# Optimization experiments

Measured on AMD Instinct MI355X. Metric: run time of the kernel, lower is better.

## Reference

```python
import jax, jax.numpy as jnp
import numpy as np

FEATURE_SIZE = (64, 64)   # (H, W)
N_REGIONS = 32
POOL = (3, 3)             # (ph, pw)
IOU_THR = 0.4
B, R, C = 4, 128, 256


def setup_inputs() -> dict:
    key = jax.random.key(0)
    kf, kx, ky, kw, kh = jax.random.split(key, 5)
    H, W = FEATURE_SIZE
    features = jax.random.normal(kf, (B, H, W, C), dtype=jnp.float32)
    # realistic RPN-style proposals in feature coordinates (x, y, w, h)
    x = jax.random.uniform(kx, (B, R), minval=0.0, maxval=W - 4.0)
    y = jax.random.uniform(ky, (B, R), minval=0.0, maxval=H - 4.0)
    w = jax.random.uniform(kw, (B, R), minval=4.0, maxval=W / 2.0)
    h = jax.random.uniform(kh, (B, R), minval=4.0, maxval=H / 2.0)
    roi = jnp.stack([x, y, w, h], axis=-1).astype(jnp.float32)
    return {"features": features, "roi": roi}


def _pairwise_iou(b):
    # b: [R, 4] xywh
    x1, y1 = b[:, 0], b[:, 1]
    x2, y2 = x1 + b[:, 2], y1 + b[:, 3]
    area = b[:, 2] * b[:, 3]
    iw = jnp.maximum(jnp.minimum(x2[:, None], x2[None, :]) - jnp.maximum(x1[:, None], x1[None, :]), 0.0)
    ih = jnp.maximum(jnp.minimum(y2[:, None], y2[None, :]) - jnp.maximum(y1[:, None], y1[None, :]), 0.0)
    inter = iw * ih
    return inter / (area[:, None] + area[None, :] - inter)


def _nms_indices(iou):
    # greedy sequential suppression: a discarded box never suppresses others
    Rn = iou.shape[0]
    j = jnp.arange(Rn)

    def body(p, keep):
        sup = keep & (j > p) & (iou[p] > IOU_THR) & keep[p]
        return keep & ~sup

    keep = jax.lax.fori_loop(0, Rn - 1, body, jnp.ones((Rn,), bool))
    # kept indices in ascending (objectness) order, padded with last index
    idx = jnp.sort(jnp.where(keep, j, Rn))[:N_REGIONS]
    return jnp.minimum(idx, Rn - 1).astype(jnp.int32)


def _clip_roi(roi):
    # roi: [B, N, 4] float xywh -> int32 [B, N, 4] xywh, clipped + min-size fixed
    H, W = FEATURE_SIZE
    x_min = jnp.maximum(0.0, roi[..., 0]).astype(jnp.int32)
    y_min = jnp.maximum(0.0, roi[..., 1]).astype(jnp.int32)
    x_max = jnp.minimum(float(W), roi[..., 0] + roi[..., 2]).astype(jnp.int32)
    y_max = jnp.minimum(float(H), roi[..., 1] + roi[..., 3]).astype(jnp.int32)

    def fix_axis(mn, mx, ps, fs):
        pad = ps - (mx - mn)
        fix_min = mn < pad // 2
        fix_max = fs - mx < (1 + pad) // 2
        sym = (pad > 0) & ~(fix_min | fix_max)
        omin = jnp.where(sym, mn - pad // 2, mn)
        omax = jnp.where(sym, mx + (1 + pad) // 2, mx)
        cmn = (pad > 0) & fix_min
        cmx = (pad > 0) & fix_max
        omin = jnp.where(cmn, 0, omin)
        omax = jnp.where(cmn, ps, omax)
        omin = jnp.where(cmx, fs - ps, omin)
        omax = jnp.where(cmx, fs, omax)
        return omin, omax

    xmn, xmx = fix_axis(x_min, x_max, POOL[1], W)
    ymn, ymx = fix_axis(y_min, y_max, POOL[0], H)
    return jnp.stack([xmn, ymn, xmx - xmn, ymx - ymn], axis=-1)


def _pool_one(feat, box):
    # feat: [H, W, C]; box: int32 [4] = (x, y, w, h); adaptive max pool to POOL
    H, W = FEATURE_SIZE
    ph, pw = POOL
    x, y, w, h = box[0], box[1], box[2], box[3]
    rows = jnp.arange(H)
    cols = jnp.arange(W)
    # cell index per row/col; last cell absorbs the remainder (matches floor steps)
    rcell = jnp.clip((rows - y) // (h // ph), 0, ph - 1)
    ccell = jnp.clip((cols - x) // (w // pw), 0, pw - 1)
    rvalid = (rows >= y) & (rows < y + h)
    cvalid = (cols >= x) & (cols < x + w)
    neg = jnp.finfo(feat.dtype).min
    f = jnp.where(rvalid[:, None, None], feat, neg)           # [H, W, C]
    rmax = jax.ops.segment_max(f, rcell, num_segments=ph)     # [ph, W, C]
    rmax = jnp.where(cvalid[None, :, None], rmax, neg)
    out = jax.ops.segment_max(jnp.swapaxes(rmax, 0, 1), ccell, num_segments=pw)  # [pw, ph, C]
    return jnp.swapaxes(out, 0, 1)                            # [ph, pw, C]


def reference(features, roi):
    iou = jax.vmap(_pairwise_iou)(roi)                         # [B, R, R]
    idx = jax.vmap(_nms_indices)(iou)                          # [B, N]
    roi_sup = jnp.take_along_axis(roi, idx[:, :, None], axis=1)  # [B, N, 4]
    roi_clipped = _clip_roi(roi_sup)                           # int32 [B, N, 4]
    pool_img = jax.vmap(_pool_one, in_axes=(None, 0))          # over regions
    pooled = jax.vmap(pool_img, in_axes=(0, 0))(features, roi_clipped)  # [B, N, ph, pw, C]
    return pooled, roi_clipped
```

## Files before the change

kernel.cpp:

```cpp
#include <hip/hip_runtime.h>
#include <float.h>

#define FH 64
#define FW 64
#define FC 256
#define NB 4
#define NR 128
#define NREG 32
#define POOLH 3
#define POOLW 3
#define IOU_THR 0.4f
#define NCELL (POOLH * POOLW)
#define MAXPIX 160

#define POOLED_ELEMS (NB * NREG * NCELL * FC)

__device__ inline void fix_axis(int mn, int mx, int ps, int fs, int& omin, int& omax) {
    int pad = ps - (mx - mn);
    bool fix_min = mn < (pad >> 1);
    bool fix_max = (fs - mx) < ((1 + pad) >> 1);
    bool sym = (pad > 0) && !(fix_min || fix_max);
    omin = sym ? (mn - (pad >> 1)) : mn;
    omax = sym ? (mx + ((1 + pad) >> 1)) : mx;
    if ((pad > 0) && fix_min) { omin = 0; omax = ps; }
    if ((pad > 0) && fix_max) { omin = fs - ps; omax = fs; }
}

__device__ inline float4 max4(float4 a, float4 b) {
    float4 o;
    o.x = fmaxf(a.x, b.x); o.y = fmaxf(a.y, b.y);
    o.z = fmaxf(a.z, b.z); o.w = fmaxf(a.w, b.w);
    return o;
}

__device__ inline unsigned long long readlane64(unsigned long long v, int lane) {
    unsigned lo = (unsigned)__builtin_amdgcn_readlane((int)(unsigned)v, lane);
    unsigned hi = (unsigned)__builtin_amdgcn_readlane((int)(unsigned)(v >> 32), lane);
    return ((unsigned long long)hi << 32) | lo;
}

__global__ __launch_bounds__(256) void fused_kernel(
    const float* __restrict__ features,
    const float* __restrict__ roi,
    float* __restrict__ out)
{
    const int hwid = blockIdx.x;
    const int b = (hwid >> 1) & 3;
    const int j = (hwid >> 3) * 2 + (hwid & 1);
    const int r = j / NCELL;
    const int cell = j - r * NCELL;
    const int ci = cell / POOLW, cj = cell - ci * POOLW;
    const int reg = b * NREG + r;
    const int tid = threadIdx.x;
    const int wid = tid >> 6;
    const int lane = tid & 63;

    __shared__ float sx1[NR], sy1[NR], sx2[NR], sy2[NR], sarea[NR];
    __shared__ unsigned long long smask[NR][2];
    __shared__ int spix[MAXPIX];
    __shared__ float4 sred[4][64];

    if (tid < NR) {
        const float4 bx = *(const float4*)(roi + ((size_t)b * NR + tid) * 4);
        sx1[tid] = bx.x; sy1[tid] = bx.y;
        sx2[tid] = bx.x + bx.z; sy2[tid] = bx.y + bx.w;
        sarea[tid] = bx.z * bx.w;
    }
    __syncthreads();

    if (wid != 1) {
        const int p = tid & 127;
        const int half = tid >> 7;
        const int j0 = half << 6;
        const float px1 = sx1[p], py1 = sy1[p], px2 = sx2[p], py2 = sy2[p], pa = sarea[p];
        unsigned long long m = 0ull;
        #pragma unroll 8
        for (int t = 0; t < 64; ++t) {
            const int jj = j0 + t;
            float iw = fmaxf(fminf(px2, sx2[jj]) - fmaxf(px1, sx1[jj]), 0.0f);
            float ih = fmaxf(fminf(py2, sy2[jj]) - fmaxf(py1, sy1[jj]), 0.0f);
            float inter = iw * ih;
            bool sup = (jj > p) && (inter > IOU_THR * (pa + sarea[jj] - inter));
            m |= ((unsigned long long)sup) << t;
        }
        smask[p][half] = m;
    }
    __syncthreads();

    const unsigned long long aLo = smask[lane][0];
    const unsigned long long aHi = smask[lane][1];
    const unsigned long long bHi = smask[lane + 64][1];

    int idx = NR - 1;
    {
        unsigned long long k1 = ~0ull;
        int cnt = 0;
        unsigned long long cur = ~0ull;
        while (cur && cnt < NREG) {
            int p = __ffsll((unsigned long long)cur) - 1;
            if (cnt == r) idx = p;
            ++cnt;
            int ps = __builtin_amdgcn_readfirstlane(p);
            unsigned long long m0 = readlane64(aLo, ps);
            unsigned long long m1 = readlane64(aHi, ps);
            cur = (cur & (cur - 1)) & ~m0;
            k1 &= ~m1;
        }
        cur = k1;
        while (cur && cnt < NREG) {
            int p = __ffsll((unsigned long long)cur) - 1;
            if (cnt == r) idx = 64 + p;
            ++cnt;
            int ps = __builtin_amdgcn_readfirstlane(p);
            unsigned long long m1 = readlane64(bHi, ps);
            cur = (cur & (cur - 1)) & ~m1;
        }
    }

    int xmn, xmx, ymn, ymx;
    {
        float x1 = sx1[idx], y1 = sy1[idx], x2f = sx2[idx], y2f = sy2[idx];
        int x_min = (int)fmaxf(0.0f, x1);
        int y_min = (int)fmaxf(0.0f, y1);
        int x_max = (int)fminf((float)FW, x2f);
        int y_max = (int)fminf((float)FH, y2f);
        fix_axis(x_min, x_max, POOLW, FW, xmn, xmx);
        fix_axis(y_min, y_max, POOLH, FH, ymn, ymx);
    }
    if (tid == 0 && cell == 0) {
        float* orc = out + POOLED_ELEMS + ((size_t)reg) * 4;
        orc[0] = (float)xmn;
        orc[1] = (float)ymn;
        orc[2] = (float)(xmx - xmn);
        orc[3] = (float)(ymx - ymn);
    }

    const int x = xmn, y = ymn, w = xmx - xmn, h = ymx - ymn;
    const int hh = h / POOLH;
    const int ww = w / POOLW;
    const int r0 = y + ci * hh;
    const int r1 = (ci < POOLH - 1) ? (y + (ci + 1) * hh) : (y + h);
    const int c0 = x + cj * ww;
    const int c1 = (cj < POOLW - 1) ? (x + (cj + 1) * ww) : (x + w);
    const int ncols = c1 - c0;
    const int n = (r1 - r0) * ncols;

    if (tid < n) {
        int q = tid / ncols;
        int cc = tid - q * ncols;
        spix[tid] = ((r0 + q) * FW + (c0 + cc)) * FC;
    }
    __syncthreads();

    const float* fbase = features + (size_t)b * FH * FW * FC;
    const float4 negv = {-FLT_MAX, -FLT_MAX, -FLT_MAX, -FLT_MAX};
    float4 m0 = negv, m1 = negv, m2 = negv, m3 = negv;
    float4 m4 = negv, m5 = negv, m6 = negv, m7 = negv;
    int k = wid;
    for (; k + 28 < n; k += 32) {
        int o0 = spix[k],      o1 = spix[k + 4],  o2 = spix[k + 8],  o3 = spix[k + 12];
        int o4 = spix[k + 16], o5 = spix[k + 20], o6 = spix[k + 24], o7 = spix[k + 28];
        float4 v0 = ((const float4*)(fbase + o0))[lane];
        float4 v1 = ((const float4*)(fbase + o1))[lane];
        float4 v2 = ((const float4*)(fbase + o2))[lane];
        float4 v3 = ((const float4*)(fbase + o3))[lane];
        float4 v4 = ((const float4*)(fbase + o4))[lane];
        float4 v5 = ((const float4*)(fbase + o5))[lane];
        float4 v6 = ((const float4*)(fbase + o6))[lane];
        float4 v7 = ((const float4*)(fbase + o7))[lane];
        m0 = max4(m0, v0); m1 = max4(m1, v1); m2 = max4(m2, v2); m3 = max4(m3, v3);
        m4 = max4(m4, v4); m5 = max4(m5, v5); m6 = max4(m6, v6); m7 = max4(m7, v7);
    }
    for (; k + 12 < n; k += 16) {
        int o0 = spix[k], o1 = spix[k + 4], o2 = spix[k + 8], o3 = spix[k + 12];
        float4 v0 = ((const float4*)(fbase + o0))[lane];
        float4 v1 = ((const float4*)(fbase + o1))[lane];
        float4 v2 = ((const float4*)(fbase + o2))[lane];
        float4 v3 = ((const float4*)(fbase + o3))[lane];
        m0 = max4(m0, v0); m1 = max4(m1, v1); m2 = max4(m2, v2); m3 = max4(m3, v3);
    }
    for (; k < n; k += 4) {
        float4 v = ((const float4*)(fbase + spix[k]))[lane];
        m0 = max4(m0, v);
    }
    m0 = max4(max4(m0, m1), max4(m2, m3));
    m4 = max4(max4(m4, m5), max4(m6, m7));
    sred[wid][lane] = max4(m0, m4);
    __syncthreads();

    if (tid < 64) {
        float4 a = max4(max4(sred[0][tid], sred[1][tid]),
                        max4(sred[2][tid], sred[3][tid]));
        float4* ob = (float4*)(out + ((size_t)reg * NCELL + cell) * FC);
        ob[tid] = a;
    }
}

extern "C" void kernel_launch(void* const* d_in, const int* in_sizes, int n_in,
                              void* d_out, int out_size, void* d_ws, size_t ws_size,
                              hipStream_t stream) {
    const float* features = (const float*)d_in[0];
    const float* roi = (const float*)d_in[1];
    float* out = (float*)d_out;
    (void)in_sizes; (void)n_in; (void)out_size; (void)d_ws; (void)ws_size;

    fused_kernel<<<NB * NREG * NCELL, 256, 0, stream>>>(features, roi, out);
}
```

Before: 82.00 us.

## Assign one pooling cell per wavefront and cut grid to 256 blocks

The kernel moves from one block per (region, cell), where all four wavefronts split that cell's pixels, to one pooling cell per wavefront, with 64 blocks per image. This cuts the number of blocks that redundantly recompute the IoU mask and NMS from 1152 to 256. Wave 0 now resolves all 32 kept boxes at once and stores the clipped boxes in shared memory. The 32 leftover cells per image go to wave 0 of the first 32 blocks. This adds load imbalance, since each wave reduces a whole cell with a 16-way unrolled gather, and occupancy falls from four times as many blocks.

```diff
diff --git a/kernel.cpp b/kernel.cpp
--- a/kernel.cpp
+++ b/kernel.cpp
@@ -11,7 +11,7 @@
 #define POOLW 3
 #define IOU_THR 0.4f
 #define NCELL (POOLH * POOLW)
-#define MAXPIX 160
+#define MAXPIX 144
 
 #define POOLED_ELEMS (NB * NREG * NCELL * FC)
 
@@ -39,7 +39,69 @@
     return ((unsigned long long)hi << 32) | lo;
 }
 
-__global__ __launch_bounds__(256) void fused_kernel(
+__device__ inline float4 pool_pixels(const float* __restrict__ fbase,
+                                     const int* spixw, int nn, int lane) {
+    const float4 negv = {-FLT_MAX, -FLT_MAX, -FLT_MAX, -FLT_MAX};
+    float4 m[16];
+    #pragma unroll
+    for (int i = 0; i < 16; ++i) m[i] = negv;
+    int k = 0;
+    for (; k + 15 < nn; k += 16) {
+        float4 v[16];
+        #pragma unroll
+        for (int i = 0; i < 16; ++i)
+            v[i] = ((const float4*)(fbase + spixw[k + i]))[lane];
+        #pragma unroll
+        for (int i = 0; i < 16; ++i) m[i] = max4(m[i], v[i]);
+    }
+    for (; k + 3 < nn; k += 4) {
+        float4 v0 = ((const float4*)(fbase + spixw[k]))[lane];
+        float4 v1 = ((const float4*)(fbase + spixw[k + 1]))[lane];
+        float4 v2 = ((const float4*)(fbase + spixw[k + 2]))[lane];
+        float4 v3 = ((const float4*)(fbase + spixw[k + 3]))[lane];
+        m[0] = max4(m[0], v0); m[1] = max4(m[1], v1);
+        m[2] = max4(m[2], v2); m[3] = max4(m[3], v3);
+    }
+    for (; k < nn; ++k)
+        m[0] = max4(m[0], ((const float4*)(fbase + spixw[k]))[lane]);
+    #pragma unroll
+    for (int s = 8; s > 0; s >>= 1)
+        for (int i = 0; i < s; ++i) m[i] = max4(m[i], m[i + s]);
+    return m[0];
+}
+
+__device__ inline void do_cell(int c, int b, const int (*sbox4)[4], int* spixw,
+                               const float* __restrict__ fbase,
+                               float* __restrict__ out, int lane) {
+    const int r = c / NCELL;
+    const int cell = c - r * NCELL;
+    const int ci = cell / POOLW, cj = cell - ci * POOLW;
+    const int x = sbox4[r][0], y = sbox4[r][1], w = sbox4[r][2], h = sbox4[r][3];
+    const int hh = h / POOLH;
+    const int ww = w / POOLW;
+    const int r0 = y + ci * hh;
+    const int r1 = (ci < POOLH - 1) ? (y + (ci + 1) * hh) : (y + h);
+    const int c0 = x + cj * ww;
+    const int c1 = (cj < POOLW - 1) ? (x + (cj + 1) * ww) : (x + w);
+    const int ncols = c1 - c0;
+    const int nn = (r1 - r0) * ncols;
+
+    for (int t = lane; t < nn; t += 64) {
+        int q = t / ncols;
+        int cc = t - q * ncols;
+        spixw[t] = ((r0 + q) * FW + (c0 + cc)) * FC;
+    }
+
+    float4 a = pool_pixels(fbase, spixw, nn, lane);
+    ((float4*)(out + ((size_t)(b * NREG + r) * NCELL + cell) * FC))[lane] = a;
+
+    if (cell == 0 && lane < 4) {
+        int v = (lane == 0) ? x : (lane == 1) ? y : (lane == 2) ? w : h;
+        out[POOLED_ELEMS + (size_t)(b * NREG + r) * 4 + lane] = (float)v;
+    }
+}
+
+__global__ __launch_bounds__(256, 1) void fused_kernel(
     const float* __restrict__ features,
     const float* __restrict__ roi,
     float* __restrict__ out)
@@ -47,18 +109,15 @@
     const int hwid = blockIdx.x;
     const int b = (hwid >> 1) & 3;
     const int j = (hwid >> 3) * 2 + (hwid & 1);
-    const int r = j / NCELL;
-    const int cell = j - r * NCELL;
-    const int ci = cell / POOLW, cj = cell - ci * POOLW;
-    const int reg = b * NREG + r;
     const int tid = threadIdx.x;
     const int wid = tid >> 6;
     const int lane = tid & 63;
+    const int g = j * 4 + wid;
 
     __shared__ float sx1[NR], sy1[NR], sx2[NR], sy2[NR], sarea[NR];
     __shared__ unsigned long long smask[NR][2];
-    __shared__ int spix[MAXPIX];
-    __shared__ float4 sred[4][64];
+    __shared__ int sbox4[NREG][4];
+    __shared__ int spix[4][MAXPIX];
 
     if (tid < NR) {
         const float4 bx = *(const float4*)(roi + ((size_t)b * NR + tid) * 4);
@@ -87,113 +146,54 @@
     }
     __syncthreads();
 
-    const unsigned long long aLo = smask[lane][0];
-    const unsigned long long aHi = smask[lane][1];
-    const unsigned long long bHi = smask[lane + 64][1];
-
-    int idx = NR - 1;
-    {
-        unsigned long long k1 = ~0ull;
-        int cnt = 0;
-        unsigned long long cur = ~0ull;
-        while (cur && cnt < NREG) {
-            int p = __ffsll((unsigned long long)cur) - 1;
-            if (cnt == r) idx = p;
-            ++cnt;
-            int ps = __builtin_amdgcn_readfirstlane(p);
-            unsigned long long m0 = readlane64(aLo, ps);
-            unsigned long long m1 = readlane64(aHi, ps);
-            cur = (cur & (cur - 1)) & ~m0;
-            k1 &= ~m1;
+    if (wid == 0) {
+        const unsigned long long aLo = smask[lane][0];
+        const unsigned long long aHi = smask[lane][1];
+        const unsigned long long bHi = smask[lane + 64][1];
+
+        int myidx = NR - 1;
+        {
+            unsigned long long k1 = ~0ull;
+            int cnt = 0;
+            unsigned long long cur = ~0ull;
+            while (cur && cnt < NREG) {
+                int p = __ffsll((unsigned long long)cur) - 1;
+                if (cnt == lane) myidx = p;
+                ++cnt;
+                int ps = __builtin_amdgcn_readfirstlane(p);
+                cur = (cur & (cur - 1)) & ~readlane64(aLo, ps);
+                k1 &= ~readlane64(aHi, ps);
+            }
+            cur = k1;
+            while (cur && cnt < NREG) {
+                int p = __ffsll((unsigned long long)cur) - 1;
+                if (cnt == lane) myidx = 64 + p;
+                ++cnt;
+                int ps = __builtin_amdgcn_readfirstlane(p);
+                cur = (cur & (cur - 1)) & ~readlane64(bHi, ps);
+            }
         }
-        cur = k1;
-        while (cur && cnt < NREG) {
-            int p = __ffsll((unsigned long long)cur) - 1;
-            if (cnt == r) idx = 64 + p;
-            ++cnt;
-            int ps = __builtin_amdgcn_readfirstlane(p);
-            unsigned long long m1 = readlane64(bHi, ps);
-            cur = (cur & (cur - 1)) & ~m1;
+        if (lane < NREG) {
+            float x1 = sx1[myidx], y1 = sy1[myidx], x2f = sx2[myidx], y2f = sy2[myidx];
+            int x_min = (int)fmaxf(0.0f, x1);
+            int y_min = (int)fmaxf(0.0f, y1);
+            int x_max = (int)fminf((float)FW, x2f);
+            int y_max = (int)fminf((float)FH, y2f);
+            int xmn, xmx, ymn, ymx;
+            fix_axis(x_min, x_max, POOLW, FW, xmn, xmx);
+            fix_axis(y_min, y_max, POOLH, FH, ymn, ymx);
+            sbox4[lane][0] = xmn;
+            sbox4[lane][1] = ymn;
+            sbox4[lane][2] = xmx - xmn;
+            sbox4[lane][3] = ymx - ymn;
         }
     }
-
-    int xmn, xmx, ymn, ymx;
-    {
-        float x1 = sx1[idx], y1 = sy1[idx], x2f = sx2[idx], y2f = sy2[idx];
-        int x_min = (int)fmaxf(0.0f, x1);
-        int y_min = (int)fmaxf(0.0f, y1);
-        int x_max = (int)fminf((float)FW, x2f);
-        int y_max = (int)fminf((float)FH, y2f);
-        fix_axis(x_min, x_max, POOLW, FW, xmn, xmx);
-        fix_axis(y_min, y_max, POOLH, FH, ymn, ymx);
-    }
-    if (tid == 0 && cell == 0) {
-        float* orc = out + POOLED_ELEMS + ((size_t)reg) * 4;
-        orc[0] = (float)xmn;
-        orc[1] = (float)ymn;
-        orc[2] = (float)(xmx - xmn);
-        orc[3] = (float)(ymx - ymn);
-    }
-
-    const int x = xmn, y = ymn, w = xmx - xmn, h = ymx - ymn;
-    const int hh = h / POOLH;
-    const int ww = w / POOLW;
-    const int r0 = y + ci * hh;
-    const int r1 = (ci < POOLH - 1) ? (y + (ci + 1) * hh) : (y + h);
-    const int c0 = x + cj * ww;
-    const int c1 = (cj < POOLW - 1) ? (x + (cj + 1) * ww) : (x + w);
-    const int ncols = c1 - c0;
-    const int n = (r1 - r0) * ncols;
-
-    if (tid < n) {
-        int q = tid / ncols;
-        int cc = tid - q * ncols;
-        spix[tid] = ((r0 + q) * FW + (c0 + cc)) * FC;
-    }
     __syncthreads();
 
     const float* fbase = features + (size_t)b * FH * FW * FC;
-    const float4 negv = {-FLT_MAX, -FLT_MAX, -FLT_MAX, -FLT_MAX};
-    float4 m0 = negv, m1 = negv, m2 = negv, m3 = negv;
-    float4 m4 = negv, m5 = negv, m6 = negv, m7 = negv;
-    int k = wid;
-    for (; k + 28 < n; k += 32) {
-        int o0 = spix[k],      o1 = spix[k + 4],  o2 = spix[k + 8],  o3 = spix[k + 12];
-        int o4 = spix[k + 16], o5 = spix[k + 20], o6 = spix[k + 24], o7 = spix[k + 28];
-        float4 v0 = ((const float4*)(fbase + o0))[lane];
-        float4 v1 = ((const float4*)(fbase + o1))[lane];
-        float4 v2 = ((const float4*)(fbase + o2))[lane];
-        float4 v3 = ((const float4*)(fbase + o3))[lane];
-        float4 v4 = ((const float4*)(fbase + o4))[lane];
-        float4 v5 = ((const float4*)(fbase + o5))[lane];
-        float4 v6 = ((const float4*)(fbase + o6))[lane];
-        float4 v7 = ((const float4*)(fbase + o7))[lane];
-        m0 = max4(m0, v0); m1 = max4(m1, v1); m2 = max4(m2, v2); m3 = max4(m3, v3);
-        m4 = max4(m4, v4); m5 = max4(m5, v5); m6 = max4(m6, v6); m7 = max4(m7, v7);
-    }
-    for (; k + 12 < n; k += 16) {
-        int o0 = spix[k], o1 = spix[k + 4], o2 = spix[k + 8], o3 = spix[k + 12];
-        float4 v0 = ((const float4*)(fbase + o0))[lane];
-        float4 v1 = ((const float4*)(fbase + o1))[lane];
-        float4 v2 = ((const float4*)(fbase + o2))[lane];
-        float4 v3 = ((const float4*)(fbase + o3))[lane];
-        m0 = max4(m0, v0); m1 = max4(m1, v1); m2 = max4(m2, v2); m3 = max4(m3, v3);
-    }
-    for (; k < n; k += 4) {
-        float4 v = ((const float4*)(fbase + spix[k]))[lane];
-        m0 = max4(m0, v);
-    }
-    m0 = max4(max4(m0, m1), max4(m2, m3));
-    m4 = max4(max4(m4, m5), max4(m6, m7));
-    sred[wid][lane] = max4(m0, m4);
-    __syncthreads();
-
-    if (tid < 64) {
-        float4 a = max4(max4(sred[0][tid], sred[1][tid]),
-                        max4(sred[2][tid], sred[3][tid]));
-        float4* ob = (float4*)(out + ((size_t)reg * NCELL + cell) * FC);
-        ob[tid] = a;
-    }
+    do_cell(g, b, sbox4, spix[wid], fbase, out, lane);
+    if (wid == 0 && j < NREG)
+        do_cell(256 + j, b, sbox4, spix[0], fbase, out, lane);
 }
 
 extern "C" void kernel_launch(void* const* d_in, const int* in_sizes, int n_in,
@@ -204,5 +204,5 @@
     float* out = (float*)d_out;
     (void)in_sizes; (void)n_in; (void)out_size; (void)d_ws; (void)ws_size;
 
-    fused_kernel<<<NB * NREG * NCELL, 256, 0, stream>>>(features, roi, out);
-}
+    fused_kernel<<<NB * 64, 256, 0, stream>>>(features, roi, out);
+}
```

Result: no change. 81.61 us (-0.5%).
